# Kernel optimization log

Measured on AMD Instinct MI355X. Metric: run time of the kernel, lower is better.

Reference implementation:

```python
import jax, jax.numpy as jnp
import numpy as np

L, B, T, D, V = 4, 32, 512, 512, 1000


def setup_inputs() -> dict:
    key = jax.random.key(0)
    k0, k1, k2, k3, k4 = jax.random.split(key, 5)
    ids = jax.random.randint(k0, (B, T), 0, V)
    mask = jax.random.randint(k1, (B, T), 0, 2).astype(bool)  # True = valid token
    emb = jax.random.normal(k2, (V, D), dtype=jnp.float32) * 0.1
    W = jax.random.normal(k3, (L, D, 3 * D), dtype=jnp.float32) / np.float32(np.sqrt(D))
    v = jax.random.normal(k4, (L, 2, D), dtype=jnp.float32) * 0.1  # (v_f, v_r) per layer
    b = jnp.zeros((L, 2, D), dtype=jnp.float32)                    # (b_f, b_r) per layer
    return {"ids": ids, "mask": mask, "emb": emb, "W": W, "v": v, "b": b}


def _sru_layer(x, pad, Wl, vf, vr, bf, br):
    # x: [T,B,D] layer input; pad: [T,B,1] bool (True = padded step)
    Tn, Bn, Dn = x.shape
    U = jnp.einsum('tbd,de->tbe', x, Wl).reshape(Tn, Bn, 3, Dn)
    xt, fpre, rpre = U[:, :, 0], U[:, :, 1], U[:, :, 2]

    def step(c, inp):
        xt_t, fp_t, rp_t, x_t, pad_t = inp
        f = jax.nn.sigmoid(fp_t + vf * c + bf)
        r = jax.nn.sigmoid(rp_t + vr * c + br)
        c_new = f * c + (1.0 - f) * xt_t
        h = r * jnp.tanh(c_new) + (1.0 - r) * x_t  # highway (input_size==hidden_size)
        c_out = jnp.where(pad_t, c, c_new)          # padded step: keep state
        h = jnp.where(pad_t, 0.0, h)                # padded step: zero output
        return c_out, h

    c0 = jnp.zeros_like(x[0])  # zero initial hidden state, as in the torch code
    _, h = jax.lax.scan(step, c0, (xt, fpre, rpre, x, pad))
    return h  # [T,B,D]


def reference(ids, mask, emb, W, v, b):
    x = emb[ids]                       # CharEmbedder lookup: [B,T,D]
    x = jnp.transpose(x, (1, 0, 2))    # [T,B,D]  (permute(1,0,2))
    pad = (~mask).T[:, :, None]        # inverted_mask.T -> [T,B,1]
    for l in range(L):
        x = _sru_layer(x, pad, W[l], v[l, 0], v[l, 1], b[l, 0], b[l, 1])
    return jnp.transpose(x, (1, 0, 2))  # back to [B,T,D]
```

## Files before the change

### kernel.cpp

```cpp
#include <hip/hip_runtime.h>
#include <hip/hip_bf16.h>


#define LAYERS 4
#define BB 32
#define TT 512
#define DD 512
#define N3 1536
#define MROWS (TT * BB)
#define WPL ((size_t)DD * N3)
#define SB 32
#define LOG2E 1.4426950408889634f
#define TWOLOG2E 2.8853900817779268f

typedef unsigned short u16;
typedef _Float16 half8 __attribute__((ext_vector_type(8)));
typedef float f32x4 __attribute__((ext_vector_type(4)));

__device__ __forceinline__ float b2f(u16 u) {
  union { unsigned int i; float f; } x;
  x.i = ((unsigned int)u) << 16;
  return x.f;
}
__device__ __forceinline__ u16 f2h(float f) {
  _Float16 h = (_Float16)f;
  return *(u16*)&h;
}
__device__ __forceinline__ float rcpf(float x) { return __builtin_amdgcn_rcpf(x); }
__device__ __forceinline__ float exp2f_(float x) { return __builtin_amdgcn_exp2f(x); }

__device__ __forceinline__ void async_ld16(const void* g, void* l) {
  __builtin_amdgcn_global_load_lds(
      (const __attribute__((address_space(1))) void*)g,
      (__attribute__((address_space(3))) void*)l, 16, 0, 0);
}
__device__ __forceinline__ void async_ld4(const void* g, void* l) {
  __builtin_amdgcn_global_load_lds(
      (const __attribute__((address_space(1))) void*)g,
      (__attribute__((address_space(3))) void*)l, 4, 0, 0);
}

__global__ void detect_kernel(const u16* __restrict__ emb_u,
                              const int* __restrict__ mask_i,
                              const int* __restrict__ ids_i,
                              int* __restrict__ flags) {
  __shared__ int cnt[3];
  __shared__ int zc;
  int tid = threadIdx.x;
  if (tid < 3) cnt[tid] = 0;
  if (tid == 0) zc = 0;
  __syncthreads();
  int bad = 0, zero_even = 0;
  for (int i = tid; i < 8192; i += 256) {
    u16 u = emb_u[i];
    unsigned e = (u >> 7) & 0xFF;
    if (e >= 0x8F) bad++;
    if ((i & 1) == 0 && u == 0) zero_even++;
  }
  if (bad) atomicAdd(&cnt[0], bad);
  if (zero_even) atomicAdd(&zc, zero_even);
  if (tid < 64) {
    unsigned vv = (unsigned)mask_i[tid];
    if (vv > 1u) atomicAdd(&cnt[1], 1);
  }
  if (tid < 256) {
    if (ids_i[2 * tid + 1] == 0) atomicAdd(&cnt[2], 1);
  }
  __syncthreads();
  if (tid == 0) {
    flags[0] = (cnt[0] > 64 || zc > 3000) ? 1 : 0;
    flags[1] = (cnt[1] > 0) ? 1 : 0;
    flags[2] = (cnt[2] >= 192) ? 1 : 0;
  }
}

__global__ __launch_bounds__(256)
void wprep_kernel(const void* __restrict__ W, u16* __restrict__ W16,
                  const int* __restrict__ flags) {
  __shared__ float tileW[32][33];
  int l = blockIdx.z;
  int k0 = blockIdx.x * 32;
  int n0 = blockIdx.y * 32;
  int tx = threadIdx.x & 31;
  int ty = threadIdx.x >> 5;
  int ff = flags[0];
  const float* Wf = (const float*)W + (size_t)l * WPL;
  const u16* Wb = (const u16*)W + (size_t)l * WPL;
  for (int kk = ty; kk < 32; kk += 8) {
    size_t off = (size_t)(k0 + kk) * N3 + n0 + tx;
    tileW[kk][tx] = ff ? Wf[off] : b2f(Wb[off]);
  }
  __syncthreads();
  u16* outP = W16 + (size_t)l * WPL;
  for (int nn = ty; nn < 32; nn += 8) {
    float x = tileW[tx][nn];
    outP[(size_t)(n0 + nn) * DD + k0 + tx] = f2h(x);
  }
}

__global__ void embed_kernel(const int* __restrict__ ids,
                             const void* __restrict__ emb,
                             float* __restrict__ X,
                             u16* __restrict__ X16,
                             const int* __restrict__ flags) {
  int i = blockIdx.x * 256 + threadIdx.x;
  int d = i & (DD - 1);
  int tb = i >> 9;
  int b = tb & (BB - 1);
  int t = tb >> 5;
  int ii = b * TT + t;
  int id = flags[2] ? ids[2 * ii] : ids[ii];
  float val = flags[0] ? ((const float*)emb)[id * DD + d]
                       : b2f(((const u16*)emb)[id * DD + d]);
  X[((size_t)b * TT + t) * DD + d] = val;
  X16[i] = f2h(val);
}

__global__ __launch_bounds__(256)
void gemm_kernel(const u16* __restrict__ X16, const u16* __restrict__ W16l,
                 const void* __restrict__ bvec, int layer,
                 const int* __restrict__ flags,
                 float* __restrict__ U, int row_base) {
  __shared__ u16 At[128][64];
  __shared__ u16 Bt[128][64];
  const int tid = threadIdx.x;
  const int row0 = blockIdx.x * 128;
  const int col0 = blockIdx.y * 128;
  const int lane = tid & 63, wave = tid >> 6;
  const int wm = (wave >> 1) * 64, wn = (wave & 1) * 64;
  const int m16 = lane & 15, quad = lane >> 4;
  const int isA = (wave < 2);
  const int rbase = (wave & 1) * 64;
  const int srow = lane >> 3;
  const int sseg = (lane & 7) ^ (srow & 7);

  f32x4 acc[4][4];
#pragma unroll
  for (int mi = 0; mi < 4; ++mi)
#pragma unroll
    for (int ni = 0; ni < 4; ++ni)
#pragma unroll
      for (int r = 0; r < 4; ++r) acc[mi][ni][r] = 0.f;

  const u16* srcBase = isA ? X16 : W16l;
  const int gbase = isA ? (row_base + row0 + rbase) : (col0 + rbase);

  for (int kv = 0; kv < 512; kv += 64) {
    __syncthreads();
    {
      const u16* src = srcBase + (size_t)(gbase + srow) * DD + kv + sseg * 8;
      u16(*dst)[64] = isA ? At : Bt;
#pragma unroll
      for (int i = 0; i < 8; ++i)
        async_ld16(src + (size_t)i * 8 * DD, &dst[rbase + i * 8][0]);
    }
    __syncthreads();

    half8 af[2][4], bfr[2][4];
#pragma unroll
    for (int kk = 0; kk < 2; ++kk)
#pragma unroll
      for (int i = 0; i < 4; ++i) {
        int ra = wm + i * 16 + m16;
        af[kk][i] = *(const half8*)&At[ra][((kk * 4 + quad) ^ (ra & 7)) * 8];
        int rb = wn + i * 16 + m16;
        bfr[kk][i] = *(const half8*)&Bt[rb][((kk * 4 + quad) ^ (rb & 7)) * 8];
      }
#pragma unroll
    for (int kk = 0; kk < 2; ++kk)
#pragma unroll
      for (int mi = 0; mi < 4; ++mi)
#pragma unroll
        for (int ni = 0; ni < 4; ++ni)
          acc[mi][ni] = __builtin_amdgcn_mfma_f32_16x16x32_f16(
              af[kk][mi], bfr[kk][ni], acc[mi][ni], 0, 0, 0);
  }

  const int ff = flags[0];
#pragma unroll
  for (int ni = 0; ni < 4; ++ni) {
    int cix = col0 + wn + ni * 16 + m16;
    int p = cix >> 9;
    int dd = cix & 511;
    float bias = 0.f;
    if (p > 0) {
      size_t bo = (size_t)layer * 2 * DD + (size_t)(p - 1) * DD + dd;
      bias = ff ? ((const float*)bvec)[bo] : b2f(((const u16*)bvec)[bo]);
    }
#pragma unroll
    for (int mi = 0; mi < 4; ++mi) {
      int r0 = row0 + wm + mi * 16 + quad * 4;
#pragma unroll
      for (int reg = 0; reg < 4; ++reg) {
        float val = acc[mi][ni][reg];
        val = (p == 0) ? val : -(val + bias) * LOG2E;
        U[(size_t)(r0 + reg) * N3 + cix] = val;
      }
    }
  }
}

template <int EMIT>
__global__ __launch_bounds__(448, 1)
void scan_kernel(const float* __restrict__ U, float* __restrict__ X,
                 u16* __restrict__ X16,
                 const void* __restrict__ mask_p, const void* __restrict__ vbase,
                 int layer, const int* __restrict__ flags,
                 float* __restrict__ carry, int t0, int nt) {
  __shared__ float bufA[2][2][SB][64];
  __shared__ float bufB[3][2][SB][64];
  __shared__ float ring[2][2][SB][64];
  __shared__ int msk[TT];
  const int tid = threadIdx.x;
  const int wave = tid >> 6, lane = tid & 63;
  const int idx0 = blockIdx.x * 64;
  const int b = idx0 >> 9;
  const int d0 = idx0 & 511;
  const int ff = flags[0], fm = flags[1];

  const int* mi_ = (const int*)mask_p + b * TT;
  const unsigned char* mb_ = (const unsigned char*)mask_p + b * TT;
  for (int i = tid; i < nt; i += 448) msk[i] = fm ? (int)mb_[t0 + i] : mi_[t0 + i];

  float vfs = 0.f, vrs = 0.f, c = 0.f;
  {
    int d = d0 + lane;
    size_t voff = (size_t)layer * 2 * DD;
    if (wave == 0) {
      float vf = ff ? ((const float*)vbase)[voff + d]
                    : b2f(((const u16*)vbase)[voff + d]);
      vfs = -vf * LOG2E;
      c = (t0 == 0) ? 0.f : carry[idx0 + lane];
    } else if (wave >= 1 && wave <= 4) {
      float vr = ff ? ((const float*)vbase)[voff + DD + d]
                    : b2f(((const u16*)vbase)[voff + DD + d]);
      vrs = -vr * LOG2E;
    }
  }

  const int nbuf = nt / SB;

  auto produceA = [&](int k) {
    int ph = k & 1, tl = k * SB;
    const float* u0 = U + ((size_t)tl * BB + b) * N3 + d0 + lane;
#pragma unroll
    for (int s = 0; s < SB; ++s)
      async_ld4(u0 + (size_t)s * BB * N3, &bufA[ph][0][s][0]);
#pragma unroll
    for (int s = 0; s < SB; ++s)
      async_ld4(u0 + 512 + (size_t)s * BB * N3, &bufA[ph][1][s][0]);
  };
  auto produceB = [&](int k) {
    int ph = k % 3, tl = k * SB;
    const float* u2 = U + ((size_t)tl * BB + b) * N3 + 1024 + d0 + lane;
    const float* xb = X + ((size_t)b * TT + t0 + tl) * DD + d0 + lane;
#pragma unroll
    for (int s = 0; s < SB; ++s)
      async_ld4(u2 + (size_t)s * BB * N3, &bufB[ph][0][s][0]);
#pragma unroll
    for (int s = 0; s < SB; ++s)
      async_ld4(xb + (size_t)s * DD, &bufB[ph][1][s][0]);
  };

  float* Xp = X + (size_t)b * TT * DD + d0 + lane;

  auto hphase = [&](int j, int hw) {
    int phc = j & 1, phb = j % 3;
    int sbase = hw * (SB / 4);
#pragma unroll
    for (int si = 0; si < SB / 4; ++si) {
      int s = sbase + si;
      float cprev = ring[phc][0][s][lane];
      float cn = ring[phc][1][s][lane];
      float rps = bufB[phb][0][s][lane];
      float xin = bufB[phb][1][s][lane];
      int m = msk[j * SB + s];
      float tr = exp2f_(fmaf(vrs, cprev, rps));
      float r = rcpf(1.f + tr);
      float e2 = exp2f_(cn * TWOLOG2E);
      float th = fmaf(-2.f, rcpf(e2 + 1.f), 1.f);
      float h = fmaf(r, th - xin, xin);
      float hout = (m == 0) ? 0.f : h;
      int tg = t0 + j * SB + s;
      Xp[(size_t)tg * DD] = hout;
      if (EMIT)
        X16[((size_t)tg * BB + b) * DD + d0 + lane] = f2h(hout);
    }
  };

  if (wave == 5) produceA(0);
  if (wave == 6) produceB(0);

  for (int k = 0; k < nbuf; ++k) {
    __syncthreads();
    if (wave == 5) {
      if (k + 1 < nbuf) produceA(k + 1);
    } else if (wave == 6) {
      if (k + 1 < nbuf) produceB(k + 1);
    } else if (wave == 0) {
      int ph = k & 1;
#pragma unroll 8
      for (int s = 0; s < SB; ++s) {
        float xt = bufA[ph][0][s][lane];
        float fps = bufA[ph][1][s][lane];
        float t = exp2f_(fmaf(vfs, c, fps));
        float f = rcpf(1.f + t);
        float cn = fmaf(f, c - xt, xt);
        ring[ph][0][s][lane] = c;
        ring[ph][1][s][lane] = cn;
        c = (msk[k * SB + s] == 0) ? c : cn;
      }
    } else {
      if (k > 0) hphase(k - 1, wave - 1);
    }
  }
  __syncthreads();
  if (wave >= 1 && wave <= 4) hphase(nbuf - 1, wave - 1);
  if (wave == 0) carry[idx0 + lane] = c;
}

__global__ void sentinel_kernel(float* out) { out[threadIdx.x] = 12345.f; }

extern "C" void kernel_launch(void* const* d_in, const int* in_sizes, int n_in,
                              void* d_out, int out_size, void* d_ws, size_t ws_size,
                              hipStream_t stream) {
  const int* ids = (const int*)d_in[0];
  const void* mask = d_in[1];
  const void* emb = d_in[2];
  const void* W = d_in[3];
  const void* v = d_in[4];
  const void* bp = d_in[5];

  char* ws = (char*)d_ws;
  int* flags = (int*)ws;
  float* carry = (float*)(ws + 4096);
  const size_t offX16 = 69632;
  const size_t offW16 = offX16 + (size_t)MROWS * DD * 2;
  const size_t offU = offW16 + (size_t)LAYERS * WPL * 2;
  const size_t perT = (size_t)BB * N3 * 4;

  const int cand[4] = {512, 256, 128, 64};
  int chunkT = 0;
  for (int i = 0; i < 4; ++i) {
    if (ws_size >= offU + (size_t)cand[i] * perT) { chunkT = cand[i]; break; }
  }
  if (!chunkT) {
    sentinel_kernel<<<1, 256, 0, stream>>>((float*)d_out);
    return;
  }

  u16* X16 = (u16*)(ws + offX16);
  u16* W16 = (u16*)(ws + offW16);
  float* U = (float*)(ws + offU);
  float* X = (float*)d_out;

  detect_kernel<<<1, 256, 0, stream>>>((const u16*)emb, (const int*)mask,
                                       (const int*)ids, flags);
  wprep_kernel<<<dim3(16, 48, 4), 256, 0, stream>>>(W, W16, flags);
  embed_kernel<<<MROWS * DD / 256, 256, 0, stream>>>(ids, emb, X, X16, flags);

  int nch = TT / chunkT;
  for (int l = 0; l < LAYERS; ++l) {
    const u16* W16l = W16 + (size_t)l * WPL;
    for (int ch = 0; ch < nch; ++ch) {
      int t0 = ch * chunkT;
      dim3 g(chunkT * BB / 128, N3 / 128);
      gemm_kernel<<<g, 256, 0, stream>>>(X16, W16l, bp, l, flags, U, t0 * BB);
      if (l < LAYERS - 1)
        scan_kernel<1><<<BB * DD / 64, 448, 0, stream>>>(U, X, X16, mask, v, l,
                                                         flags, carry, t0, chunkT);
      else
        scan_kernel<0><<<BB * DD / 64, 448, 0, stream>>>(U, X, X16, mask, v, l,
                                                         flags, carry, t0, chunkT);
    }
  }
}
```

Baseline: 414.6 us.

## Store GEMM pre-activations in fp16 planar layout and drop fp32 intermediates

The GEMM now writes its output U as fp16 in three planar [chunkM,512] slabs instead of interleaved fp32. The scan reads these, and the highway input, through paired 4-byte async loads into fp16 LDS buffers and converts them in registers. Intermediate layers write only the fp16 X16 activations, and the embed kernel no longer writes fp32 X, so fp32 output is stored only by the last layer. This roughly halves the bytes moved between the GEMM and the scan, at the cost of fp16 rounding on the gate pre-activations and the highway input.

```diff
diff --git a/kernel.cpp b/kernel.cpp
--- a/kernel.cpp
+++ b/kernel.cpp
@@ -14,6 +14,7 @@
 #define TWOLOG2E 2.8853900817779268f
 
 typedef unsigned short u16;
+typedef unsigned int u32;
 typedef _Float16 half8 __attribute__((ext_vector_type(8)));
 typedef float f32x4 __attribute__((ext_vector_type(4)));
 
@@ -25,6 +26,11 @@
 __device__ __forceinline__ u16 f2h(float f) {
   _Float16 h = (_Float16)f;
   return *(u16*)&h;
+}
+__device__ __forceinline__ float h2f(u16 u) {
+  _Float16 h;
+  *(u16*)&h = u;
+  return (float)h;
 }
 __device__ __forceinline__ float rcpf(float x) { return __builtin_amdgcn_rcpf(x); }
 __device__ __forceinline__ float exp2f_(float x) { return __builtin_amdgcn_exp2f(x); }
@@ -100,7 +106,6 @@
 
 __global__ void embed_kernel(const int* __restrict__ ids,
                              const void* __restrict__ emb,
-                             float* __restrict__ X,
                              u16* __restrict__ X16,
                              const int* __restrict__ flags) {
   int i = blockIdx.x * 256 + threadIdx.x;
@@ -112,7 +117,6 @@
   int id = flags[2] ? ids[2 * ii] : ids[ii];
   float val = flags[0] ? ((const float*)emb)[id * DD + d]
                        : b2f(((const u16*)emb)[id * DD + d]);
-  X[((size_t)b * TT + t) * DD + d] = val;
   X16[i] = f2h(val);
 }
 
@@ -120,7 +124,7 @@
 void gemm_kernel(const u16* __restrict__ X16, const u16* __restrict__ W16l,
                  const void* __restrict__ bvec, int layer,
                  const int* __restrict__ flags,
-                 float* __restrict__ U, int row_base) {
+                 u16* __restrict__ U16, int row_base, int chunkM) {
   __shared__ u16 At[128][64];
   __shared__ u16 Bt[128][64];
   const int tid = threadIdx.x;
@@ -187,6 +191,7 @@
       size_t bo = (size_t)layer * 2 * DD + (size_t)(p - 1) * DD + dd;
       bias = ff ? ((const float*)bvec)[bo] : b2f(((const u16*)bvec)[bo]);
     }
+    u16* up = U16 + (size_t)p * chunkM * 512;
 #pragma unroll
     for (int mi = 0; mi < 4; ++mi) {
       int r0 = row0 + wm + mi * 16 + quad * 4;
@@ -194,7 +199,7 @@
       for (int reg = 0; reg < 4; ++reg) {
         float val = acc[mi][ni][reg];
         val = (p == 0) ? val : -(val + bias) * LOG2E;
-        U[(size_t)(r0 + reg) * N3 + cix] = val;
+        up[(size_t)(r0 + reg) * 512 + dd] = f2h(val);
       }
     }
   }
@@ -202,13 +207,13 @@
 
 template <int EMIT>
 __global__ __launch_bounds__(448, 1)
-void scan_kernel(const float* __restrict__ U, float* __restrict__ X,
+void scan_kernel(const u16* __restrict__ U16, float* __restrict__ X,
                  u16* __restrict__ X16,
                  const void* __restrict__ mask_p, const void* __restrict__ vbase,
                  int layer, const int* __restrict__ flags,
-                 float* __restrict__ carry, int t0, int nt) {
-  __shared__ float bufA[2][2][SB][64];
-  __shared__ float bufB[3][2][SB][64];
+                 float* __restrict__ carry, int t0, int nt, int chunkM) {
+  __shared__ u16 bufA[2][2][SB][64];
+  __shared__ u16 bufB[3][2][SB][64];
   __shared__ float ring[2][2][SB][64];
   __shared__ int msk[TT];
   const int tid = threadIdx.x;
@@ -240,26 +245,38 @@
 
   const int nbuf = nt / SB;
 
+  auto ld_pair = [&](const u16* rowS, const u16* rowS1, void* ldst) {
+    const u32* a0 = (const u32*)rowS;
+    const u32* a1 = (const u32*)rowS1;
+    const u32* ga = (lane < 32) ? (a0 + lane) : (a1 + (lane - 32));
+    async_ld4(ga, ldst);
+  };
+
   auto produceA = [&](int k) {
     int ph = k & 1, tl = k * SB;
-    const float* u0 = U + ((size_t)tl * BB + b) * N3 + d0 + lane;
-#pragma unroll
-    for (int s = 0; s < SB; ++s)
-      async_ld4(u0 + (size_t)s * BB * N3, &bufA[ph][0][s][0]);
-#pragma unroll
-    for (int s = 0; s < SB; ++s)
-      async_ld4(u0 + 512 + (size_t)s * BB * N3, &bufA[ph][1][s][0]);
+    const u16* p0 = U16 + ((size_t)tl * BB + b) * 512 + d0;
+    const u16* p1 = p0 + (size_t)chunkM * 512;
+#pragma unroll
+    for (int s = 0; s < SB; s += 2)
+      ld_pair(p0 + (size_t)s * BB * 512, p0 + (size_t)(s + 1) * BB * 512,
+              &bufA[ph][0][s][0]);
+#pragma unroll
+    for (int s = 0; s < SB; s += 2)
+      ld_pair(p1 + (size_t)s * BB * 512, p1 + (size_t)(s + 1) * BB * 512,
+              &bufA[ph][1][s][0]);
   };
   auto produceB = [&](int k) {
     int ph = k % 3, tl = k * SB;
-    const float* u2 = U + ((size_t)tl * BB + b) * N3 + 1024 + d0 + lane;
-    const float* xb = X + ((size_t)b * TT + t0 + tl) * DD + d0 + lane;
-#pragma unroll
-    for (int s = 0; s < SB; ++s)
-      async_ld4(u2 + (size_t)s * BB * N3, &bufB[ph][0][s][0]);
-#pragma unroll
-    for (int s = 0; s < SB; ++s)
-      async_ld4(xb + (size_t)s * DD, &bufB[ph][1][s][0]);
+    const u16* p2 = U16 + 2 * (size_t)chunkM * 512 + ((size_t)tl * BB + b) * 512 + d0;
+    const u16* xb = X16 + ((size_t)(t0 + tl) * BB + b) * DD + d0;
+#pragma unroll
+    for (int s = 0; s < SB; s += 2)
+      ld_pair(p2 + (size_t)s * BB * 512, p2 + (size_t)(s + 1) * BB * 512,
+              &bufB[ph][0][s][0]);
+#pragma unroll
+    for (int s = 0; s < SB; s += 2)
+      ld_pair(xb + (size_t)s * BB * DD, xb + (size_t)(s + 1) * BB * DD,
+              &bufB[ph][1][s][0]);
   };
 
   float* Xp = X + (size_t)b * TT * DD + d0 + lane;
@@ -272,8 +289,8 @@
       int s = sbase + si;
       float cprev = ring[phc][0][s][lane];
       float cn = ring[phc][1][s][lane];
-      float rps = bufB[phb][0][s][lane];
-      float xin = bufB[phb][1][s][lane];
+      float rps = h2f(bufB[phb][0][s][lane]);
+      float xin = h2f(bufB[phb][1][s][lane]);
       int m = msk[j * SB + s];
       float tr = exp2f_(fmaf(vrs, cprev, rps));
       float r = rcpf(1.f + tr);
@@ -282,9 +299,10 @@
       float h = fmaf(r, th - xin, xin);
       float hout = (m == 0) ? 0.f : h;
       int tg = t0 + j * SB + s;
-      Xp[(size_t)tg * DD] = hout;
       if (EMIT)
         X16[((size_t)tg * BB + b) * DD + d0 + lane] = f2h(hout);
+      else
+        Xp[(size_t)tg * DD] = hout;
     }
   };
 
@@ -301,8 +319,8 @@
       int ph = k & 1;
 #pragma unroll 8
       for (int s = 0; s < SB; ++s) {
-        float xt = bufA[ph][0][s][lane];
-        float fps = bufA[ph][1][s][lane];
+        float xt = h2f(bufA[ph][0][s][lane]);
+        float fps = h2f(bufA[ph][1][s][lane]);
         float t = exp2f_(fmaf(vfs, c, fps));
         float f = rcpf(1.f + t);
         float cn = fmaf(f, c - xt, xt);
@@ -337,7 +355,7 @@
   const size_t offX16 = 69632;
   const size_t offW16 = offX16 + (size_t)MROWS * DD * 2;
   const size_t offU = offW16 + (size_t)LAYERS * WPL * 2;
-  const size_t perT = (size_t)BB * N3 * 4;
+  const size_t perT = (size_t)BB * N3 * 2;
 
   const int cand[4] = {512, 256, 128, 64};
   int chunkT = 0;
@@ -348,16 +366,17 @@
     sentinel_kernel<<<1, 256, 0, stream>>>((float*)d_out);
     return;
   }
+  const int chunkM = chunkT * BB;
 
   u16* X16 = (u16*)(ws + offX16);
   u16* W16 = (u16*)(ws + offW16);
-  float* U = (float*)(ws + offU);
+  u16* U16 = (u16*)(ws + offU);
   float* X = (float*)d_out;
 
   detect_kernel<<<1, 256, 0, stream>>>((const u16*)emb, (const int*)mask,
                                        (const int*)ids, flags);
   wprep_kernel<<<dim3(16, 48, 4), 256, 0, stream>>>(W, W16, flags);
-  embed_kernel<<<MROWS * DD / 256, 256, 0, stream>>>(ids, emb, X, X16, flags);
+  embed_kernel<<<MROWS * DD / 256, 256, 0, stream>>>(ids, emb, X16, flags);
 
   int nch = TT / chunkT;
   for (int l = 0; l < LAYERS; ++l) {
@@ -365,13 +384,16 @@
     for (int ch = 0; ch < nch; ++ch) {
       int t0 = ch * chunkT;
       dim3 g(chunkT * BB / 128, N3 / 128);
-      gemm_kernel<<<g, 256, 0, stream>>>(X16, W16l, bp, l, flags, U, t0 * BB);
+      gemm_kernel<<<g, 256, 0, stream>>>(X16, W16l, bp, l, flags, U16,
+                                         t0 * BB, chunkM);
       if (l < LAYERS - 1)
-        scan_kernel<1><<<BB * DD / 64, 448, 0, stream>>>(U, X, X16, mask, v, l,
-                                                         flags, carry, t0, chunkT);
+        scan_kernel<1><<<BB * DD / 64, 448, 0, stream>>>(U16, X, X16, mask, v, l,
+                                                         flags, carry, t0, chunkT,
+                                                         chunkM);
       else
-        scan_kernel<0><<<BB * DD / 64, 448, 0, stream>>>(U, X, X16, mask, v, l,
-                                                         flags, carry, t0, chunkT);
-    }
-  }
-}
+        scan_kernel<0><<<BB * DD / 64, 448, 0, stream>>>(U16, X, X16, mask, v, l,
+                                                         flags, carry, t0, chunkT,
+                                                         chunkM);
+    }
+  }
+}
```

After: 346.5 us. 16.4% less time.
